# Optimization experiments

Measured on AMD Instinct MI355X. Metric: run time of the kernel, lower is better.

Reference implementation:

```python
import jax, jax.numpy as jnp
import numpy as np

EPSILON = 1e-06
REG_STRENGTH = 1.0
KL_FACTOR = 1.0
N_CLASSES = 4
Z_DIM = 32
G_EMBED = 2
N_GROUPS = 16
N_FREQS = 64
N_ROIS = 32
BATCH = 1024


def setup_inputs() -> dict:
    key = jax.random.key(0)
    ks = jax.random.split(key, 16)
    n_feat = N_FREQS * N_ROIS * N_ROIS
    features = jax.random.normal(ks[0], (BATCH, N_FREQS, N_ROIS, N_ROIS), dtype=jnp.float32)
    labels = jax.random.randint(ks[1], (BATCH,), 0, N_CLASSES)
    groups = jax.random.randint(ks[2], (BATCH,), 0, N_GROUPS)
    weights = jax.random.uniform(ks[3], (BATCH,), dtype=jnp.float32)
    noise = jax.random.normal(ks[4], (BATCH, Z_DIM), dtype=jnp.float32)
    # learned parameters (torch Linear weights stored as [in, out])
    s1 = 1.0 / np.sqrt(n_feat + G_EMBED)
    group_embed = jax.random.normal(ks[5], (N_GROUPS, G_EMBED), dtype=jnp.float32)
    W1 = jax.random.uniform(ks[6], (n_feat + G_EMBED, Z_DIM), minval=-s1, maxval=s1, dtype=jnp.float32)
    b1 = jax.random.uniform(ks[7], (Z_DIM,), minval=-s1, maxval=s1, dtype=jnp.float32)
    W2 = jax.random.uniform(ks[8], (n_feat + G_EMBED, Z_DIM), minval=-s1, maxval=s1, dtype=jnp.float32)
    b2 = jax.random.uniform(ks[9], (Z_DIM,), minval=-s1, maxval=s1, dtype=jnp.float32)
    freq_factors = jax.random.normal(ks[10], (N_GROUPS, Z_DIM, N_FREQS), dtype=jnp.float32)
    roi_1_factors = jax.random.normal(ks[11], (N_GROUPS, Z_DIM, N_ROIS), dtype=jnp.float32)
    roi_2_factors = jax.random.normal(ks[12], (N_GROUPS, Z_DIM, N_ROIS), dtype=jnp.float32)
    s2 = 1.0 / np.sqrt(Z_DIM)
    lin_W = jax.random.uniform(ks[13], (Z_DIM, Z_DIM), minval=-s2, maxval=s2, dtype=jnp.float32)
    lin_b = jax.random.uniform(ks[14], (Z_DIM,), minval=-s2, maxval=s2, dtype=jnp.float32)
    logit_bias = jnp.zeros((1, N_CLASSES), dtype=jnp.float32)
    return {
        "features": features, "labels": labels, "groups": groups, "weights": weights,
        "noise": noise, "group_embed": group_embed, "W1": W1, "b1": b1, "W2": W2, "b2": b2,
        "freq_factors": freq_factors, "roi_1_factors": roi_1_factors,
        "roi_2_factors": roi_2_factors, "lin_W": lin_W, "lin_b": lin_b,
        "logit_bias": logit_bias,
    }


def reference(features, labels, groups, weights, noise, group_embed, W1, b1, W2, b2,
              freq_factors, roi_1_factors, roi_2_factors, lin_W, lin_b, logit_bias):
    b = features.shape[0]
    flat = features.reshape(b, -1)                               # [b, f*r*r]
    aug = jnp.concatenate([flat, group_embed[groups]], axis=1)   # [b, nfeat+e]
    z_mu = aug @ W1 + b1                                         # [b, z]
    z_log_std = aug @ W2 + b2
    sigma = EPSILON + jnp.exp(z_log_std)
    # KL(N(mu, sigma) || N(0, 1)), summed over z
    kld = jnp.sum(-jnp.log(sigma) + 0.5 * (sigma * sigma + z_mu * z_mu - 1.0), axis=1)
    zs = z_mu + sigma * noise                                    # rsample
    zs = zs @ lin_W + lin_b
    # CP reconstruction with softplus-positive factors
    freq_f = jax.nn.softplus(freq_factors)                       # [g, z, f]
    roi_1_f = jax.nn.softplus(roi_1_factors)                     # [g, z, r]
    roi_2_f = jax.nn.softplus(roi_2_factors)
    freq_loss = jnp.var(freq_f, axis=0, ddof=1).mean(axis=1).sum()
    roi_loss = (jnp.var(roi_1_f, axis=0, ddof=1) + jnp.var(roi_2_f, axis=0, ddof=1)).mean(axis=1).sum()
    volume = jnp.einsum('bz,bzf,bzr,bzs->bfrs', jax.nn.softplus(zs),
                        freq_f[groups], roi_1_f[groups], roi_2_f[groups])
    rec_loss = REG_STRENGTH * jnp.mean((flat - volume.reshape(b, -1)) ** 2, axis=1)
    logits = jnp.concatenate([zs[:, :N_CLASSES - 1], jnp.ones((b, 1), zs.dtype)], axis=1) + logit_bias
    log_probs = jax.nn.log_softmax(logits, axis=1)[jnp.arange(b), labels]
    loss = jnp.mean(rec_loss - weights * log_probs + KL_FACTOR * kld) + freq_loss + roi_loss
    return loss
```

## Files before the change

### kernel.cpp

```cpp
#include <hip/hip_runtime.h>
#include <math.h>

#define NFEAT 65536
#define KS1   32
#define NTILE 32

#define WS_Z     0
#define WS_T     65536
#define WS_SS    98304
#define WS_SCAL  99328
#define WS_FSP   99392
#define WS_R1SP  132160
#define WS_R2SP  148544
#define WS_G     164928
#define WS_LOSSB 181312
#define WS_SORTI 182336
#define WS_FT    184832
#define WS_R1T   217600
#define WS_WP    233984

typedef __bf16 bf16x8 __attribute__((ext_vector_type(8)));
typedef float  floatx4 __attribute__((ext_vector_type(4)));

__device__ __forceinline__ float softplusf(float x) {
    return fmaxf(x, 0.f) + log1pf(expf(-fabsf(x)));
}

__device__ __forceinline__ void glds16(const void* g, void* l) {
    __builtin_amdgcn_global_load_lds(
        (const __attribute__((address_space(1))) unsigned int*)g,
        (__attribute__((address_space(3))) unsigned int*)l, 16, 0, 0);
}

__global__ __launch_bounds__(256) void k0a(const float* __restrict__ ff,
                                           const float* __restrict__ r1,
                                           const float* __restrict__ r2,
                                           const float* __restrict__ W1,
                                           const float* __restrict__ W2,
                                           const int* __restrict__ groups,
                                           float* __restrict__ ws) {
    const int bid = blockIdx.x, t = threadIdx.x;
    __shared__ int cnt[16], pos[16];
    if (bid < 256) {
        int i = bid * 256 + t;
        if (i < 32768) {
            float sp = softplusf(ff[i]);
            ws[WS_FSP + i] = sp;
            int g = i >> 11, z = (i >> 6) & 31, f = i & 63;
            ws[WS_FT + g * 2048 + f * 32 + z] = sp;
        } else if (i < 49152) {
            int ii = i - 32768;
            float sp = softplusf(r1[ii]);
            ws[WS_R1SP + ii] = sp;
            int g = ii >> 10, z = (ii >> 5) & 31, r = ii & 31;
            ws[WS_R1T + g * 1024 + r * 32 + z] = sp;
        } else {
            int ii = i - 49152;
            ws[WS_R2SP + ii] = softplusf(r2[ii]);
        }
    } else if (bid < 2304) {
        int e = (bid - 256) * 256 + t;
        int kg = e >> 6, col = e & 63;
        const float* Wsrc = (col < 32 ? W1 : W2) + (size_t)kg * 256 + (col & 31);
        bf16x8 o;
        #pragma unroll
        for (int j = 0; j < 8; j++) o[j] = (__bf16)Wsrc[j * 32];
        *(bf16x8*)((__bf16*)(ws + WS_WP) + (size_t)e * 8) = o;
    } else {
        int* order = (int*)(ws + WS_SORTI);
        int* tg = order + 2048; int* tb = order + 2080; int* tc = order + 2112;
        if (t < 16) cnt[t] = 0;
        __syncthreads();
        for (int i = t; i < 1024; i += 256) atomicAdd(&cnt[groups[i]], 1);
        __syncthreads();
        if (t == 0) {
            int tt = 0, base = 0;
            for (int g = 0; g < 16; g++) {
                pos[g] = base;
                int c = cnt[g];
                int nt = (c + 63) >> 6;
                for (int j = 0; j < nt; j++) {
                    tg[tt] = g; tb[tt] = base + j * 64;
                    int rem = c - j * 64;
                    tc[tt] = rem < 64 ? rem : 64;
                    tt++;
                }
                base += c;
            }
            for (; tt < NTILE; tt++) { tg[tt] = 0; tb[tt] = 0; tc[tt] = 0; }
        }
        __syncthreads();
        for (int i = t; i < 1024; i += 256) {
            int s = atomicAdd(&pos[groups[i]], 1);
            order[s] = i;
        }
        for (int i = 1024 + t; i < 2048; i += 256) order[i] = 0;
    }
}

__global__ __launch_bounds__(256) void k0b(float* __restrict__ ws) {
    __shared__ float red[256];
    __shared__ float Fg[2048], R1g[1024], R2g[1024];
    const int bid = blockIdx.x, t = threadIdx.x;
    if (bid < 12) {
        int gid = bid * 256 + t;
        float contrib = 0.f;
        if (gid < 2048) {
            const float* F = ws + WS_FSP + gid;
            float sx = 0.f, sx2 = 0.f;
            #pragma unroll
            for (int g = 0; g < 16; g++) { float x = F[g * 2048]; sx += x; sx2 += x * x; }
            contrib = (sx2 - sx * sx * (1.f / 16.f)) * (1.f / 15.f) * (1.f / 64.f);
        } else {
            int p = gid - 2048;
            const float* A = ws + WS_R1SP + p;
            const float* B = ws + WS_R2SP + p;
            float sx = 0.f, sx2 = 0.f, tx = 0.f, tx2 = 0.f;
            #pragma unroll
            for (int g = 0; g < 16; g++) {
                float x = A[g * 1024]; sx += x; sx2 += x * x;
                float y = B[g * 1024]; tx += y; tx2 += y * y;
            }
            contrib = ((sx2 - sx * sx * (1.f / 16.f)) + (tx2 - tx * tx * (1.f / 16.f)))
                      * (1.f / 15.f) * (1.f / 32.f);
        }
        red[t] = contrib;
        __syncthreads();
        for (int o = 128; o > 0; o >>= 1) {
            if (t < o) red[t] += red[t + o];
            __syncthreads();
        }
        if (t == 0) atomicAdd(ws + WS_SCAL + (bid < 8 ? 0 : 1), red[0]);
    } else {
        int g = bid - 12;
        for (int i = t; i < 2048; i += 256) Fg[i] = ws[WS_FSP + g * 2048 + i];
        for (int i = t; i < 1024; i += 256) {
            R1g[i] = ws[WS_R1SP + g * 1024 + i];
            R2g[i] = ws[WS_R2SP + g * 1024 + i];
        }
        __syncthreads();
        for (int p = t; p < 1024; p += 256) {
            int z1 = p >> 5, z2 = p & 31;
            float dF = 0.f;
            for (int f = 0; f < 64; f++) dF += Fg[z1 * 64 + f] * Fg[z2 * 64 + f];
            float d1 = 0.f, d2 = 0.f;
            for (int r = 0; r < 32; r++) {
                d1 += R1g[z1 * 32 + r] * R1g[z2 * 32 + r];
                d2 += R2g[z1 * 32 + r] * R2g[z2 * 32 + r];
            }
            ws[WS_G + g * 1024 + p] = dF * d1 * d2;
        }
    }
}

__global__ __launch_bounds__(256) void k_fused(const float* __restrict__ feat,
                                               float* __restrict__ wsf) {
    const int rt = blockIdx.x, ks = blockIdx.y;
    const int* order = (const int*)(wsf + WS_SORTI);
    const int tcnt = order[2112 + rt];
    if (tcnt == 0) return;
    const int g     = order[2048 + rt];
    const int tbase = order[2080 + rt];

    __shared__ __bf16 Bsm[2][12800];
    const int tid = threadIdx.x;
    const int w = tid >> 6, lane = tid & 63;
    const int fn = lane & 15, q4 = lane >> 4;
    const size_t kbase = (size_t)ks * 2048;

    const int rowit = w * 16 + fn;
    const int bA = order[tbase + rowit];
    const float* fp = feat + (size_t)bA * NFEAT + kbase + q4 * 8;

    const int kz = tid & 31, kg8 = tid >> 5;
    const int h = kg8 >> 1;
    float r2v[16];
    {
        const float* R2g = wsf + WS_R2SP + g * 1024 + kz * 32 + (kg8 & 1) * 16;
        float4 a0 = *(const float4*)(R2g);
        float4 a1 = *(const float4*)(R2g + 4);
        float4 a2 = *(const float4*)(R2g + 8);
        float4 a3 = *(const float4*)(R2g + 12);
        r2v[0]=a0.x; r2v[1]=a0.y; r2v[2]=a0.z; r2v[3]=a0.w;
        r2v[4]=a1.x; r2v[5]=a1.y; r2v[6]=a1.z; r2v[7]=a1.w;
        r2v[8]=a2.x; r2v[9]=a2.y; r2v[10]=a2.z; r2v[11]=a2.w;
        r2v[12]=a3.x; r2v[13]=a3.y; r2v[14]=a3.z; r2v[15]=a3.w;
    }
    const float* Ftp  = wsf + WS_FT  + g * 2048 + (ks * 2) * 32 + kz;
    const float* R1tp = wsf + WS_R1T + g * 1024 + kz;

    const __bf16* wp = (const __bf16*)(wsf + WS_WP);
    const size_t kgb = (size_t)ks * 256;

    float4 rA[2][8];

    #pragma unroll
    for (int p = 0; p < 4; p++)
        glds16(wp + ((kgb + (size_t)(w * 4 + p)) * 64 + (size_t)lane) * 8,
               &Bsm[0][(w * 4 + p) * 800]);
    #pragma unroll
    for (int kq = 0; kq < 4; kq++) {
        rA[0][kq * 2]     = *(const float4*)(fp + kq * 32);
        rA[0][kq * 2 + 1] = *(const float4*)(fp + kq * 32 + 4);
    }
    float fvF = Ftp[(1 >> 3) * 32];
    float fvR = R1tp[((1 & 7) * 4 + h) * 32];
    {
        float cf = Ftp[0] * R1tp[h * 32];
        #pragma unroll
        for (int ih = 0; ih < 2; ih++) {
            bf16x8 pk;
            #pragma unroll
            for (int j = 0; j < 8; j++) pk[j] = (__bf16)(cf * r2v[ih * 8 + j]);
            *(bf16x8*)&Bsm[0][((kg8 * 2 + ih) * 100 + 64 + kz) * 8] = pk;
        }
    }
    __syncthreads();

    floatx4 acc0 = {0,0,0,0}, acc1 = {0,0,0,0}, acc2 = {0,0,0,0};
    floatx4 acc3 = {0,0,0,0}, acc4 = {0,0,0,0}, acc5 = {0,0,0,0};
    float ssl = 0.f;

    #pragma unroll 2
    for (int cc = 0; cc < 16; cc++) {
        const int cur = cc & 1, nxt = cur ^ 1;
        float nF = 0.f, nR = 0.f;
        if (cc < 15) {
            #pragma unroll
            for (int p = 0; p < 4; p++)
                glds16(wp + ((kgb + (size_t)((cc + 1) * 16 + w * 4 + p)) * 64 + (size_t)lane) * 8,
                       &Bsm[nxt][(w * 4 + p) * 800]);
            __builtin_amdgcn_sched_barrier(0);
            const float* fpn = fp + (cc + 1) * 128;
            #pragma unroll
            for (int kq = 0; kq < 4; kq++) {
                rA[nxt][kq * 2]     = *(const float4*)(fpn + kq * 32);
                rA[nxt][kq * 2 + 1] = *(const float4*)(fpn + kq * 32 + 4);
            }
            __builtin_amdgcn_sched_barrier(0);
            nF = Ftp[((cc + 2) >> 3) * 32];
            nR = R1tp[(((cc + 2) & 7) * 4 + h) * 32];
            __builtin_amdgcn_sched_barrier(0);
        }
        __builtin_amdgcn_s_setprio(1);
        #pragma unroll
        for (int kq = 0; kq < 4; kq++) {
            float4 lo = rA[cur][kq * 2], hi = rA[cur][kq * 2 + 1];
            ssl += lo.x*lo.x + lo.y*lo.y + lo.z*lo.z + lo.w*lo.w
                 + hi.x*hi.x + hi.y*hi.y + hi.z*hi.z + hi.w*hi.w;
            bf16x8 af;
            af[0]=(__bf16)lo.x; af[1]=(__bf16)lo.y; af[2]=(__bf16)lo.z; af[3]=(__bf16)lo.w;
            af[4]=(__bf16)hi.x; af[5]=(__bf16)hi.y; af[6]=(__bf16)hi.z; af[7]=(__bf16)hi.w;
            const __bf16* bb = &Bsm[cur][((kq * 4 + q4) * 100 + fn) * 8];
            bf16x8 b0 = *(const bf16x8*)(bb);
            bf16x8 b1 = *(const bf16x8*)(bb + 16 * 8);
            bf16x8 b2 = *(const bf16x8*)(bb + 32 * 8);
            bf16x8 b3 = *(const bf16x8*)(bb + 48 * 8);
            bf16x8 b4 = *(const bf16x8*)(bb + 64 * 8);
            bf16x8 b5 = *(const bf16x8*)(bb + 80 * 8);
            acc0 = __builtin_amdgcn_mfma_f32_16x16x32_bf16(af, b0, acc0, 0, 0, 0);
            acc1 = __builtin_amdgcn_mfma_f32_16x16x32_bf16(af, b1, acc1, 0, 0, 0);
            acc2 = __builtin_amdgcn_mfma_f32_16x16x32_bf16(af, b2, acc2, 0, 0, 0);
            acc3 = __builtin_amdgcn_mfma_f32_16x16x32_bf16(af, b3, acc3, 0, 0, 0);
            acc4 = __builtin_amdgcn_mfma_f32_16x16x32_bf16(af, b4, acc4, 0, 0, 0);
            acc5 = __builtin_amdgcn_mfma_f32_16x16x32_bf16(af, b5, acc5, 0, 0, 0);
        }
        __builtin_amdgcn_s_setprio(0);
        if (cc < 15) {
            float cf = fvF * fvR;
            #pragma unroll
            for (int ih = 0; ih < 2; ih++) {
                bf16x8 pk;
                #pragma unroll
                for (int j = 0; j < 8; j++) pk[j] = (__bf16)(cf * r2v[ih * 8 + j]);
                *(bf16x8*)&Bsm[nxt][((kg8 * 2 + ih) * 100 + 64 + kz) * 8] = pk;
            }
            fvF = nF; fvR = nR;
            asm volatile("s_waitcnt vmcnt(10) lgkmcnt(0)" ::: "memory");
            __builtin_amdgcn_sched_barrier(0);
            __builtin_amdgcn_s_barrier();
        }
    }

    float ssv = ssl + __shfl_xor(ssl, 16, 64);
    ssv += __shfl_xor(ssv, 32, 64);
    if (q4 == 0 && rowit < tcnt) atomicAdd(wsf + WS_SS + bA, ssv);

    #pragma unroll
    for (int r = 0; r < 4; r++) {
        int rit = w * 16 + q4 * 4 + r;
        if (rit < tcnt) {
            int b = order[tbase + rit];
            atomicAdd(wsf + WS_Z + b * 64 +  0 + fn, acc0[r]);
            atomicAdd(wsf + WS_Z + b * 64 + 16 + fn, acc1[r]);
            atomicAdd(wsf + WS_Z + b * 64 + 32 + fn, acc2[r]);
            atomicAdd(wsf + WS_Z + b * 64 + 48 + fn, acc3[r]);
            atomicAdd(wsf + WS_T + b * 32 +  0 + fn, acc4[r]);
            atomicAdd(wsf + WS_T + b * 32 + 16 + fn, acc5[r]);
        }
    }
}

__global__ __launch_bounds__(64) void k3_batch(const float* __restrict__ W1,
                                               const float* __restrict__ W2,
                                               const float* __restrict__ b1,
                                               const float* __restrict__ b2,
                                               const float* __restrict__ gemb,
                                               const float* __restrict__ noise,
                                               const float* __restrict__ linW,
                                               const float* __restrict__ linb,
                                               const float* __restrict__ lbias,
                                               const int* __restrict__ groups,
                                               const int* __restrict__ labels,
                                               const float* __restrict__ weights,
                                               float* __restrict__ ws) {
    const int b = blockIdx.x;
    const int t = threadIdx.x;
    const int g = groups[b];
    float sum = ws[WS_Z + b * 64 + t];

    __shared__ float s_mu[32], s_sig[32], s_zs0[32], s_zs[32], s_P[32], s_red[96];
    float ge0 = gemb[g * 2], ge1 = gemb[g * 2 + 1];
    if (t < 32) {
        s_mu[t] = sum + ge0 * W1[(size_t)65536 * 32 + t] + ge1 * W1[(size_t)65537 * 32 + t] + b1[t];
    } else {
        int c = t - 32;
        float ls = sum + ge0 * W2[(size_t)65536 * 32 + c] + ge1 * W2[(size_t)65537 * 32 + c] + b2[c];
        s_sig[c] = 1e-6f + expf(ls);
    }
    __syncthreads();
    if (t < 32) s_zs0[t] = s_mu[t] + s_sig[t] * noise[b * 32 + t];
    __syncthreads();
    if (t < 32) {
        float d = linb[t];
        for (int i = 0; i < 32; i++) d = fmaf(s_zs0[i], linW[i * 32 + t], d);
        s_zs[t] = d;
        s_P[t] = softplusf(d);
    }
    __syncthreads();
    if (t < 32) {
        float mu = s_mu[t], sg = s_sig[t];
        float kld = -logf(sg) + 0.5f * (sg * sg + mu * mu - 1.f);
        float pt = s_P[t] * ws[WS_T + b * 32 + t];
        const float* Grow = ws + WS_G + g * 1024 + t * 32;
        float gd = 0.f;
        for (int j = 0; j < 32; j++) gd = fmaf(Grow[j], s_P[j], gd);
        s_red[t] = kld; s_red[32 + t] = pt; s_red[64 + t] = s_P[t] * gd;
    }
    __syncthreads();
    if (t == 0) {
        float kld = 0.f, pt = 0.f, pgp = 0.f;
        for (int i = 0; i < 32; i++) { kld += s_red[i]; pt += s_red[32 + i]; pgp += s_red[64 + i]; }
        float rec = (ws[WS_SS + b] - 2.f * pt + pgp) * (1.f / 65536.f);
        float l0 = s_zs[0] + lbias[0], l1 = s_zs[1] + lbias[1];
        float l2 = s_zs[2] + lbias[2], l3 = 1.f + lbias[3];
        float m = fmaxf(fmaxf(l0, l1), fmaxf(l2, l3));
        float lse = m + logf(expf(l0 - m) + expf(l1 - m) + expf(l2 - m) + expf(l3 - m));
        int lb = labels[b];
        float ll = ((lb == 0) ? l0 : (lb == 1) ? l1 : (lb == 2) ? l2 : l3) - lse;
        ws[WS_LOSSB + b] = rec - weights[b] * ll + kld;
    }
}

__global__ __launch_bounds__(256) void k4_final(const float* __restrict__ ws, float* __restrict__ out) {
    __shared__ float red[256];
    int t = threadIdx.x;
    float s = 0.f;
    for (int i = t; i < 1024; i += 256) s += ws[WS_LOSSB + i];
    red[t] = s;
    __syncthreads();
    for (int o = 128; o > 0; o >>= 1) {
        if (t < o) red[t] += red[t + o];
        __syncthreads();
    }
    if (t == 0) out[0] = red[0] * (1.f / 1024.f) + ws[WS_SCAL] + ws[WS_SCAL + 1];
}

extern "C" void kernel_launch(void* const* d_in, const int* in_sizes, int n_in,
                              void* d_out, int out_size, void* d_ws, size_t ws_size,
                              hipStream_t stream) {
    const float* feat    = (const float*)d_in[0];
    const int*   labels  = (const int*)d_in[1];
    const int*   groups  = (const int*)d_in[2];
    const float* weights = (const float*)d_in[3];
    const float* noise   = (const float*)d_in[4];
    const float* gemb    = (const float*)d_in[5];
    const float* W1      = (const float*)d_in[6];
    const float* b1      = (const float*)d_in[7];
    const float* W2      = (const float*)d_in[8];
    const float* b2      = (const float*)d_in[9];
    const float* ff      = (const float*)d_in[10];
    const float* r1f     = (const float*)d_in[11];
    const float* r2f     = (const float*)d_in[12];
    const float* linW    = (const float*)d_in[13];
    const float* linb    = (const float*)d_in[14];
    const float* lbias   = (const float*)d_in[15];
    float* ws = (float*)d_ws;
    float* out = (float*)d_out;

    hipMemsetAsync(ws, 0, 99392 * sizeof(float), stream);

    k0a<<<2305, 256, 0, stream>>>(ff, r1f, r2f, W1, W2, groups, ws);
    k0b<<<28, 256, 0, stream>>>(ws);
    k_fused<<<dim3(NTILE, KS1), 256, 0, stream>>>(feat, ws);
    k3_batch<<<1024, 64, 0, stream>>>(W1, W2, b1, b2, gemb, noise, linW, linb, lbias,
                                      groups, labels, weights, ws);
    k4_final<<<1, 256, 0, stream>>>(ws, out);
}
```

Baseline: 460.5 us.

## Generate CP factor B-fragments in registers instead of staging through LDS

The fused GEMM kernel no longer writes the per-group CP reconstruction factor (freq*roi1*roi2) into shared memory each chunk. Each lane now builds its own bf16 B fragments for the last two MFMA column tiles directly from preloaded softplus factors. This removes an LDS write and read per chunk, shrinks shared memory to an unpadded layout, and drops the transposed factor copies from the prep kernel. It also adds a launch-bounds occupancy hint of 4 blocks per SM. The cost is extra VALU multiplies and conversions inside the MFMA loop, plus higher register pressure. The unpadded LDS layout may also cause bank conflicts.

```diff
diff --git a/kernel.cpp b/kernel.cpp
--- a/kernel.cpp
+++ b/kernel.cpp
@@ -44,16 +44,10 @@
     if (bid < 256) {
         int i = bid * 256 + t;
         if (i < 32768) {
-            float sp = softplusf(ff[i]);
-            ws[WS_FSP + i] = sp;
-            int g = i >> 11, z = (i >> 6) & 31, f = i & 63;
-            ws[WS_FT + g * 2048 + f * 32 + z] = sp;
+            ws[WS_FSP + i] = softplusf(ff[i]);
         } else if (i < 49152) {
             int ii = i - 32768;
-            float sp = softplusf(r1[ii]);
-            ws[WS_R1SP + ii] = sp;
-            int g = ii >> 10, z = (ii >> 5) & 31, r = ii & 31;
-            ws[WS_R1T + g * 1024 + r * 32 + z] = sp;
+            ws[WS_R1SP + ii] = softplusf(r1[ii]);
         } else {
             int ii = i - 49152;
             ws[WS_R2SP + ii] = softplusf(r2[ii]);
@@ -153,8 +147,8 @@
     }
 }
 
-__global__ __launch_bounds__(256) void k_fused(const float* __restrict__ feat,
-                                               float* __restrict__ wsf) {
+__global__ __launch_bounds__(256, 4) void k_fused(const float* __restrict__ feat,
+                                                  float* __restrict__ wsf) {
     const int rt = blockIdx.x, ks = blockIdx.y;
     const int* order = (const int*)(wsf + WS_SORTI);
     const int tcnt = order[2112 + rt];
@@ -162,7 +156,7 @@
     const int g     = order[2048 + rt];
     const int tbase = order[2080 + rt];
 
-    __shared__ __bf16 Bsm[2][12800];
+    __shared__ __bf16 Bsm[2][16][512];
     const int tid = threadIdx.x;
     const int w = tid >> 6, lane = tid & 63;
     const int fn = lane & 15, q4 = lane >> 4;
@@ -172,49 +166,32 @@
     const int bA = order[tbase + rowit];
     const float* fp = feat + (size_t)bA * NFEAT + kbase + q4 * 8;
 
-    const int kz = tid & 31, kg8 = tid >> 5;
-    const int h = kg8 >> 1;
-    float r2v[16];
-    {
-        const float* R2g = wsf + WS_R2SP + g * 1024 + kz * 32 + (kg8 & 1) * 16;
-        float4 a0 = *(const float4*)(R2g);
-        float4 a1 = *(const float4*)(R2g + 4);
-        float4 a2 = *(const float4*)(R2g + 8);
-        float4 a3 = *(const float4*)(R2g + 12);
-        r2v[0]=a0.x; r2v[1]=a0.y; r2v[2]=a0.z; r2v[3]=a0.w;
-        r2v[4]=a1.x; r2v[5]=a1.y; r2v[6]=a1.z; r2v[7]=a1.w;
-        r2v[8]=a2.x; r2v[9]=a2.y; r2v[10]=a2.z; r2v[11]=a2.w;
-        r2v[12]=a3.x; r2v[13]=a3.y; r2v[14]=a3.z; r2v[15]=a3.w;
-    }
-    const float* Ftp  = wsf + WS_FT  + g * 2048 + (ks * 2) * 32 + kz;
-    const float* R1tp = wsf + WS_R1T + g * 1024 + kz;
+    float2 fva = *(const float2*)(wsf + WS_FSP + g * 2048 + fn * 64 + ks * 2);
+    float2 fvb = *(const float2*)(wsf + WS_FSP + g * 2048 + (fn + 16) * 64 + ks * 2);
+    float4 r2a0 = *(const float4*)(wsf + WS_R2SP + g * 1024 + fn * 32 + q4 * 8);
+    float4 r2a1 = *(const float4*)(wsf + WS_R2SP + g * 1024 + fn * 32 + q4 * 8 + 4);
+    float4 r2b0 = *(const float4*)(wsf + WS_R2SP + g * 1024 + (fn + 16) * 32 + q4 * 8);
+    float4 r2b1 = *(const float4*)(wsf + WS_R2SP + g * 1024 + (fn + 16) * 32 + q4 * 8 + 4);
+    const float* R1a = wsf + WS_R1SP + g * 1024 + fn * 32;
+    const float* R1b = wsf + WS_R1SP + g * 1024 + (fn + 16) * 32;
 
     const __bf16* wp = (const __bf16*)(wsf + WS_WP);
     const size_t kgb = (size_t)ks * 256;
 
     float4 rA[2][8];
+    float4 r1a[2], r1b[2];
 
     #pragma unroll
     for (int p = 0; p < 4; p++)
         glds16(wp + ((kgb + (size_t)(w * 4 + p)) * 64 + (size_t)lane) * 8,
-               &Bsm[0][(w * 4 + p) * 800]);
+               &Bsm[0][w * 4 + p][0]);
     #pragma unroll
     for (int kq = 0; kq < 4; kq++) {
         rA[0][kq * 2]     = *(const float4*)(fp + kq * 32);
         rA[0][kq * 2 + 1] = *(const float4*)(fp + kq * 32 + 4);
     }
-    float fvF = Ftp[(1 >> 3) * 32];
-    float fvR = R1tp[((1 & 7) * 4 + h) * 32];
-    {
-        float cf = Ftp[0] * R1tp[h * 32];
-        #pragma unroll
-        for (int ih = 0; ih < 2; ih++) {
-            bf16x8 pk;
-            #pragma unroll
-            for (int j = 0; j < 8; j++) pk[j] = (__bf16)(cf * r2v[ih * 8 + j]);
-            *(bf16x8*)&Bsm[0][((kg8 * 2 + ih) * 100 + 64 + kz) * 8] = pk;
-        }
-    }
+    r1a[0] = *(const float4*)(R1a);
+    r1b[0] = *(const float4*)(R1b);
     __syncthreads();
 
     floatx4 acc0 = {0,0,0,0}, acc1 = {0,0,0,0}, acc2 = {0,0,0,0};
@@ -224,12 +201,11 @@
     #pragma unroll 2
     for (int cc = 0; cc < 16; cc++) {
         const int cur = cc & 1, nxt = cur ^ 1;
-        float nF = 0.f, nR = 0.f;
         if (cc < 15) {
             #pragma unroll
             for (int p = 0; p < 4; p++)
                 glds16(wp + ((kgb + (size_t)((cc + 1) * 16 + w * 4 + p)) * 64 + (size_t)lane) * 8,
-                       &Bsm[nxt][(w * 4 + p) * 800]);
+                       &Bsm[nxt][w * 4 + p][0]);
             __builtin_amdgcn_sched_barrier(0);
             const float* fpn = fp + (cc + 1) * 128;
             #pragma unroll
@@ -238,10 +214,14 @@
                 rA[nxt][kq * 2 + 1] = *(const float4*)(fpn + kq * 32 + 4);
             }
             __builtin_amdgcn_sched_barrier(0);
-            nF = Ftp[((cc + 2) >> 3) * 32];
-            nR = R1tp[(((cc + 2) & 7) * 4 + h) * 32];
+            r1a[nxt] = *(const float4*)(R1a + ((cc + 1) & 7) * 4);
+            r1b[nxt] = *(const float4*)(R1b + ((cc + 1) & 7) * 4);
             __builtin_amdgcn_sched_barrier(0);
         }
+        const float fA = (cc & 8) ? fva.y : fva.x;
+        const float fB = (cc & 8) ? fvb.y : fvb.x;
+        const float r1av[4] = {r1a[cur].x, r1a[cur].y, r1a[cur].z, r1a[cur].w};
+        const float r1bv[4] = {r1b[cur].x, r1b[cur].y, r1b[cur].z, r1b[cur].w};
         __builtin_amdgcn_s_setprio(1);
         #pragma unroll
         for (int kq = 0; kq < 4; kq++) {
@@ -251,13 +231,22 @@
             bf16x8 af;
             af[0]=(__bf16)lo.x; af[1]=(__bf16)lo.y; af[2]=(__bf16)lo.z; af[3]=(__bf16)lo.w;
             af[4]=(__bf16)hi.x; af[5]=(__bf16)hi.y; af[6]=(__bf16)hi.z; af[7]=(__bf16)hi.w;
-            const __bf16* bb = &Bsm[cur][((kq * 4 + q4) * 100 + fn) * 8];
+            const __bf16* bb = &Bsm[cur][kq * 4 + q4][fn * 8];
             bf16x8 b0 = *(const bf16x8*)(bb);
-            bf16x8 b1 = *(const bf16x8*)(bb + 16 * 8);
-            bf16x8 b2 = *(const bf16x8*)(bb + 32 * 8);
-            bf16x8 b3 = *(const bf16x8*)(bb + 48 * 8);
-            bf16x8 b4 = *(const bf16x8*)(bb + 64 * 8);
-            bf16x8 b5 = *(const bf16x8*)(bb + 80 * 8);
+            bf16x8 b1 = *(const bf16x8*)(bb + 128);
+            bf16x8 b2 = *(const bf16x8*)(bb + 256);
+            bf16x8 b3 = *(const bf16x8*)(bb + 384);
+            float cfA = fA * r1av[kq];
+            float cfB = fB * r1bv[kq];
+            bf16x8 b4, b5;
+            b4[0]=(__bf16)(cfA*r2a0.x); b4[1]=(__bf16)(cfA*r2a0.y);
+            b4[2]=(__bf16)(cfA*r2a0.z); b4[3]=(__bf16)(cfA*r2a0.w);
+            b4[4]=(__bf16)(cfA*r2a1.x); b4[5]=(__bf16)(cfA*r2a1.y);
+            b4[6]=(__bf16)(cfA*r2a1.z); b4[7]=(__bf16)(cfA*r2a1.w);
+            b5[0]=(__bf16)(cfB*r2b0.x); b5[1]=(__bf16)(cfB*r2b0.y);
+            b5[2]=(__bf16)(cfB*r2b0.z); b5[3]=(__bf16)(cfB*r2b0.w);
+            b5[4]=(__bf16)(cfB*r2b1.x); b5[5]=(__bf16)(cfB*r2b1.y);
+            b5[6]=(__bf16)(cfB*r2b1.z); b5[7]=(__bf16)(cfB*r2b1.w);
             acc0 = __builtin_amdgcn_mfma_f32_16x16x32_bf16(af, b0, acc0, 0, 0, 0);
             acc1 = __builtin_amdgcn_mfma_f32_16x16x32_bf16(af, b1, acc1, 0, 0, 0);
             acc2 = __builtin_amdgcn_mfma_f32_16x16x32_bf16(af, b2, acc2, 0, 0, 0);
@@ -267,15 +256,6 @@
         }
         __builtin_amdgcn_s_setprio(0);
         if (cc < 15) {
-            float cf = fvF * fvR;
-            #pragma unroll
-            for (int ih = 0; ih < 2; ih++) {
-                bf16x8 pk;
-                #pragma unroll
-                for (int j = 0; j < 8; j++) pk[j] = (__bf16)(cf * r2v[ih * 8 + j]);
-                *(bf16x8*)&Bsm[nxt][((kg8 * 2 + ih) * 100 + 64 + kz) * 8] = pk;
-            }
-            fvF = nF; fvR = nR;
             asm volatile("s_waitcnt vmcnt(10) lgkmcnt(0)" ::: "memory");
             __builtin_amdgcn_sched_barrier(0);
             __builtin_amdgcn_s_barrier();
```

New measurement: 1.066 ms. +131.5%, slower.
